# Kernel optimization log

Measured on AMD Instinct MI355X. Metric: run time of the kernel, lower is better.

The kernel has to match this reference:

```python
import jax, jax.numpy as jnp
import numpy as np

N_NODES = 50000
N_EDGES = 800000
D_IN = 128
D_OUT = 128


def setup_inputs() -> dict:
    key = jax.random.key(0)
    k1, k2, k3, k4, k5 = jax.random.split(key, 5)
    x = jax.random.normal(k1, (N_NODES, D_IN), dtype=jnp.float32)
    src = jax.random.randint(k2, (N_EDGES,), 0, N_NODES, dtype=jnp.int32)
    dst = jax.random.randint(k3, (N_EDGES,), 0, N_NODES, dtype=jnp.int32)
    # nn.Linear(in_feats, out_feats): weight [out, in], bias [out]
    W = jax.random.normal(k4, (D_OUT, D_IN), dtype=jnp.float32) / np.sqrt(D_IN)
    b = jax.random.normal(k5, (D_OUT,), dtype=jnp.float32) * 0.01
    return {"x": x, "src": src, "dst": dst, "W": W, "b": b}


def reference(x, src, dst, W, b):
    # copy_u('h','m') + sum reduce: h_dst = sum_{e:(u->v)} x[u]
    msgs = x[src]  # [E, D_IN] gather of source features
    h = jax.ops.segment_sum(msgs, dst, num_segments=N_NODES)  # [N, D_IN]
    # linear: h @ W.T + b ; dropout_rate=0.0 -> identity
    out = jnp.einsum('nd,od->no', h, W) + b
    return out
```

## Files before the change

kernel.cpp:

```cpp
#include <hip/hip_runtime.h>

#define N_NODES 50000
#define N_EDGES 800000
#define D 128
#define NB 782
#define SORT_CAP 2048

typedef __attribute__((ext_vector_type(8))) short bf16x8;
typedef __attribute__((ext_vector_type(4))) float floatx4;

__device__ __forceinline__ unsigned short f2bf(float f) {
  unsigned u = __builtin_bit_cast(unsigned, f);
  unsigned r = u + 0x7FFFu + ((u >> 16) & 1u);
  return (unsigned short)(r >> 16);
}
__device__ __forceinline__ float bf2f_lo(unsigned u) {
  return __builtin_bit_cast(float, u << 16);
}
__device__ __forceinline__ float bf2f_hi(unsigned u) {
  return __builtin_bit_cast(float, u & 0xFFFF0000u);
}

#define LDA 136
#define BIN_T 256
#define BIN_CHUNK 2048
#define BIN_BLOCKS 391

struct BinShm {
  unsigned stage[BIN_CHUNK];
  unsigned short stageb[BIN_CHUNK];
  int hcnt[NB];
  int hstart[NB];
  int hcur[NB];
  int hgbase[NB];
  int wsums[4];
  int tot;
};
struct GemmShm {
  unsigned short As[64 * LDA];
  unsigned short Ws[128 * LDA];
};
union PrepShm {
  BinShm bin;
  GemmShm gemm;
};

__global__ __launch_bounds__(256) void prep_kernel(
    const float* __restrict__ x, const float* __restrict__ W,
    unsigned short* __restrict__ y,
    const int* __restrict__ src, const int* __restrict__ dst,
    int* __restrict__ bcursor, unsigned* __restrict__ ebuf, int cap) {
  __shared__ PrepShm shm;
  int t = threadIdx.x;

  if (blockIdx.x < NB) {
    unsigned short* As = shm.gemm.As;
    unsigned short* Ws = shm.gemm.Ws;
    int row0 = blockIdx.x * 64;

    for (int i = t; i < 2048; i += 256) {
      int r = i >> 5;
      int c4 = (i & 31) * 4;
      int gr = row0 + r;
      float4 v = (gr < N_NODES) ? *(const float4*)(x + (size_t)gr * D + c4)
                                : float4{0.f, 0.f, 0.f, 0.f};
      unsigned short* p = &As[r * LDA + c4];
      p[0] = f2bf(v.x); p[1] = f2bf(v.y); p[2] = f2bf(v.z); p[3] = f2bf(v.w);
    }
    for (int i = t; i < 4096; i += 256) {
      int r = i >> 5;
      int c4 = (i & 31) * 4;
      float4 wv = *(const float4*)(W + (size_t)r * D + c4);
      unsigned short* q = &Ws[r * LDA + c4];
      q[0] = f2bf(wv.x); q[1] = f2bf(wv.y); q[2] = f2bf(wv.z); q[3] = f2bf(wv.w);
    }
    __syncthreads();

    int w = t >> 6;
    int lane = t & 63;
    int ln = lane & 15;
    int quad = lane >> 4;

    floatx4 acc[8];
#pragma unroll
    for (int n = 0; n < 8; ++n) acc[n] = floatx4{0.f, 0.f, 0.f, 0.f};

#pragma unroll
    for (int ks = 0; ks < 4; ++ks) {
      int kc = ks * 32 + quad * 8;
      bf16x8 a = *(const bf16x8*)&As[(w * 16 + ln) * LDA + kc];
#pragma unroll
      for (int n = 0; n < 8; ++n) {
        bf16x8 bf = *(const bf16x8*)&Ws[(n * 16 + ln) * LDA + kc];
        acc[n] = __builtin_amdgcn_mfma_f32_16x16x32_bf16(a, bf, acc[n], 0, 0, 0);
      }
    }

    int gr0 = row0 + w * 16 + quad * 4;
#pragma unroll
    for (int n = 0; n < 8; ++n) {
      int gc = n * 16 + ln;
#pragma unroll
      for (int r = 0; r < 4; ++r) {
        int gr = gr0 + r;
        if (gr < N_NODES) y[(size_t)gr * D + gc] = f2bf(acc[n][r]);
      }
    }
  } else {
    BinShm& B = shm.bin;
    int blk = blockIdx.x - NB;
    int e0 = blk * BIN_CHUNK;
    for (int i = t; i < NB; i += BIN_T) B.hcnt[i] = 0;
    __syncthreads();

    unsigned pk[8];
    short bk[8];
#pragma unroll
    for (int j = 0; j < 8; ++j) {
      int e = e0 + j * BIN_T + t;
      bk[j] = -1;
      if (e < N_EDGES) {
        int d = dst[e];
        int s = src[e];
        pk[j] = ((unsigned)s << 6) | (unsigned)(d & 63);
        bk[j] = (short)(d >> 6);
        atomicAdd(&B.hcnt[d >> 6], 1);
      }
    }
    __syncthreads();

    int c4[4];
    int s4 = 0;
    int base4 = t * 4;
#pragma unroll
    for (int j = 0; j < 4; ++j) {
      int idx = base4 + j;
      c4[j] = (idx < NB) ? B.hcnt[idx] : 0;
      s4 += c4[j];
    }
    int incl = s4;
    int lane = t & 63, wid = t >> 6;
#pragma unroll
    for (int off = 1; off < 64; off <<= 1) {
      int n = __shfl_up(incl, off);
      if (lane >= off) incl += n;
    }
    if (lane == 63) B.wsums[wid] = incl;
    __syncthreads();
    int wbase = 0;
    for (int w2 = 0; w2 < wid; ++w2) wbase += B.wsums[w2];
    int run = wbase + incl - s4;
#pragma unroll
    for (int j = 0; j < 4; ++j) {
      int idx = base4 + j;
      if (idx < NB) { B.hstart[idx] = run; B.hcur[idx] = run; }
      run += c4[j];
    }
    if (t == BIN_T - 1) B.tot = run;
    __syncthreads();

    for (int i = t; i < NB; i += BIN_T) {
      int c = B.hcnt[i];
      B.hgbase[i] = c ? atomicAdd(&bcursor[i * 16], c) : 0;
    }
#pragma unroll
    for (int j = 0; j < 8; ++j) {
      if (bk[j] >= 0) {
        int p = atomicAdd(&B.hcur[bk[j]], 1);
        B.stage[p] = pk[j];
        B.stageb[p] = (unsigned short)bk[j];
      }
    }
    __syncthreads();

    int tot = B.tot;
    for (int i = t; i < tot; i += BIN_T) {
      int b = B.stageb[i];
      int g = B.hgbase[b] + (i - B.hstart[b]);
      if (g < cap) ebuf[(size_t)b * cap + g] = B.stage[i];
    }
  }
}

__global__ __launch_bounds__(256) void gather_sorted(
    const unsigned short* __restrict__ y, const unsigned* __restrict__ ebuf,
    const int* __restrict__ bcursor, const float* __restrict__ bias,
    float* __restrict__ out, int cap) {
  __shared__ int cnts[64];
  __shared__ int curs[64];
  __shared__ int starts[65];
  __shared__ int sorted[SORT_CAP];

  int b = blockIdx.x;
  int t = threadIdx.x;
  if (t < 64) cnts[t] = 0;
  __syncthreads();

  int cnt = bcursor[b * 16];
  if (cnt > cap) cnt = cap;
  if (cnt > SORT_CAP) cnt = SORT_CAP;
  const unsigned* eb = ebuf + (size_t)b * cap;

  for (int i = t; i < cnt; i += 256) atomicAdd(&cnts[eb[i] & 63u], 1);
  __syncthreads();

  if (t < 64) {
    int c = cnts[t];
    int v = c;
#pragma unroll
    for (int off = 1; off < 64; off <<= 1) {
      int n = __shfl_up(v, off);
      if (t >= off) v += n;
    }
    starts[t] = v - c;
    curs[t] = v - c;
    if (t == 63) starts[64] = v;
  }
  __syncthreads();

  for (int i = t; i < cnt; i += 256) {
    unsigned u = eb[i];
    int p = atomicAdd(&curs[u & 63u], 1);
    sorted[p] = (int)(u >> 6);
  }
  __syncthreads();

  int wv = t >> 6;
  int lane = t & 63;
  int g = lane >> 4;
  int l = lane & 15;
  for (int n = wv; n < 64; n += 4) {
    int node = b * 64 + n;
    int beg = starts[n];
    int end = starts[n + 1];
    float acc[8] = {0.f, 0.f, 0.f, 0.f, 0.f, 0.f, 0.f, 0.f};
    int i = beg + g;
    for (; i + 12 < end; i += 16) {
      int s0 = sorted[i];
      int s1 = sorted[i + 4];
      int s2 = sorted[i + 8];
      int s3 = sorted[i + 12];
      uint4 u0 = *(const uint4*)(y + (size_t)s0 * D + l * 8);
      uint4 u1 = *(const uint4*)(y + (size_t)s1 * D + l * 8);
      uint4 u2 = *(const uint4*)(y + (size_t)s2 * D + l * 8);
      uint4 u3 = *(const uint4*)(y + (size_t)s3 * D + l * 8);
      acc[0] += (bf2f_lo(u0.x) + bf2f_lo(u1.x)) + (bf2f_lo(u2.x) + bf2f_lo(u3.x));
      acc[1] += (bf2f_hi(u0.x) + bf2f_hi(u1.x)) + (bf2f_hi(u2.x) + bf2f_hi(u3.x));
      acc[2] += (bf2f_lo(u0.y) + bf2f_lo(u1.y)) + (bf2f_lo(u2.y) + bf2f_lo(u3.y));
      acc[3] += (bf2f_hi(u0.y) + bf2f_hi(u1.y)) + (bf2f_hi(u2.y) + bf2f_hi(u3.y));
      acc[4] += (bf2f_lo(u0.z) + bf2f_lo(u1.z)) + (bf2f_lo(u2.z) + bf2f_lo(u3.z));
      acc[5] += (bf2f_hi(u0.z) + bf2f_hi(u1.z)) + (bf2f_hi(u2.z) + bf2f_hi(u3.z));
      acc[6] += (bf2f_lo(u0.w) + bf2f_lo(u1.w)) + (bf2f_lo(u2.w) + bf2f_lo(u3.w));
      acc[7] += (bf2f_hi(u0.w) + bf2f_hi(u1.w)) + (bf2f_hi(u2.w) + bf2f_hi(u3.w));
    }
    for (; i < end; i += 4) {
      int s = sorted[i];
      uint4 u = *(const uint4*)(y + (size_t)s * D + l * 8);
      acc[0] += bf2f_lo(u.x); acc[1] += bf2f_hi(u.x);
      acc[2] += bf2f_lo(u.y); acc[3] += bf2f_hi(u.y);
      acc[4] += bf2f_lo(u.z); acc[5] += bf2f_hi(u.z);
      acc[6] += bf2f_lo(u.w); acc[7] += bf2f_hi(u.w);
    }
#pragma unroll
    for (int j = 0; j < 8; ++j) {
      acc[j] += __shfl_xor(acc[j], 16);
      acc[j] += __shfl_xor(acc[j], 32);
    }
    if (g == 0 && node < N_NODES) {
      const float* bp = bias + l * 8;
      float4 r0 = {acc[0] + bp[0], acc[1] + bp[1], acc[2] + bp[2], acc[3] + bp[3]};
      float4 r1 = {acc[4] + bp[4], acc[5] + bp[5], acc[6] + bp[6], acc[7] + bp[7]};
      float* op = out + (size_t)node * D + l * 8;
      *(float4*)op = r0;
      *(float4*)(op + 4) = r1;
    }
  }
}

__global__ __launch_bounds__(256) void hist_kernel(
    const int* __restrict__ dst, int* __restrict__ counts) {
  int e = blockIdx.x * 256 + threadIdx.x;
  if (e < N_EDGES) atomicAdd(&counts[dst[e]], 1);
}

#define SBLK 196
__global__ __launch_bounds__(256) void reduce_kernel(
    const int* __restrict__ counts, int* __restrict__ blockSums) {
  int i = blockIdx.x * 256 + threadIdx.x;
  int v = (i < N_NODES) ? counts[i] : 0;
#pragma unroll
  for (int off = 32; off; off >>= 1) v += __shfl_down(v, off);
  __shared__ int ws[4];
  int lane = threadIdx.x & 63, wid = threadIdx.x >> 6;
  if (lane == 0) ws[wid] = v;
  __syncthreads();
  if (threadIdx.x == 0) blockSums[blockIdx.x] = ws[0] + ws[1] + ws[2] + ws[3];
}

__global__ __launch_bounds__(256) void scan_kernel2(
    const int* __restrict__ counts, const int* __restrict__ blockSums,
    int* __restrict__ offsets, int* __restrict__ cursor) {
  int b = blockIdx.x;
  int t = threadIdx.x;
  int lane = t & 63, wid = t >> 6;
  int pv = (t < b) ? blockSums[t] : 0;
#pragma unroll
  for (int off = 32; off; off >>= 1) pv += __shfl_down(pv, off);
  __shared__ int ws[4];
  __shared__ int wsum[4];
  __shared__ int base_s;
  if (lane == 0) ws[wid] = pv;
  __syncthreads();
  if (t == 0) base_s = ws[0] + ws[1] + ws[2] + ws[3];
  int i = b * 256 + t;
  int c = (i < N_NODES) ? counts[i] : 0;
  int v = c;
#pragma unroll
  for (int off = 1; off < 64; off <<= 1) {
    int n = __shfl_up(v, off);
    if (lane >= off) v += n;
  }
  if (lane == 63) wsum[wid] = v;
  __syncthreads();
  int wbase = 0;
  for (int w2 = 0; w2 < wid; ++w2) wbase += wsum[w2];
  int excl = base_s + wbase + v - c;
  if (i < N_NODES) {
    offsets[i] = excl;
    cursor[i] = excl;
    if (i == N_NODES - 1) offsets[N_NODES] = excl + c;
  }
}

__global__ __launch_bounds__(256) void fill_kernel(
    const int* __restrict__ src, const int* __restrict__ dst,
    int* __restrict__ cursor, int* __restrict__ esrc) {
  int e = blockIdx.x * 256 + threadIdx.x;
  if (e >= N_EDGES) return;
  int pos = atomicAdd(&cursor[dst[e]], 1);
  esrc[pos] = src[e];
}

__global__ __launch_bounds__(256) void gemm_xw(
    const float* __restrict__ x, const float* __restrict__ W,
    unsigned short* __restrict__ y) {
  __shared__ unsigned short As[64 * LDA];
  __shared__ unsigned short Ws[128 * LDA];
  int t = threadIdx.x;
  int row0 = blockIdx.x * 64;
  for (int i = t; i < 2048; i += 256) {
    int r = i >> 5;
    int c4 = (i & 31) * 4;
    int gr = row0 + r;
    float4 v = (gr < N_NODES) ? *(const float4*)(x + (size_t)gr * D + c4)
                              : float4{0.f, 0.f, 0.f, 0.f};
    unsigned short* p = &As[r * LDA + c4];
    p[0] = f2bf(v.x); p[1] = f2bf(v.y); p[2] = f2bf(v.z); p[3] = f2bf(v.w);
  }
  for (int i = t; i < 4096; i += 256) {
    int r = i >> 5;
    int c4 = (i & 31) * 4;
    float4 wv = *(const float4*)(W + (size_t)r * D + c4);
    unsigned short* q = &Ws[r * LDA + c4];
    q[0] = f2bf(wv.x); q[1] = f2bf(wv.y); q[2] = f2bf(wv.z); q[3] = f2bf(wv.w);
  }
  __syncthreads();
  int w = t >> 6;
  int lane = t & 63;
  int ln = lane & 15;
  int quad = lane >> 4;
  floatx4 acc[8];
#pragma unroll
  for (int n = 0; n < 8; ++n) acc[n] = floatx4{0.f, 0.f, 0.f, 0.f};
#pragma unroll
  for (int ks = 0; ks < 4; ++ks) {
    int kc = ks * 32 + quad * 8;
    bf16x8 a = *(const bf16x8*)&As[(w * 16 + ln) * LDA + kc];
#pragma unroll
    for (int n = 0; n < 8; ++n) {
      bf16x8 bf = *(const bf16x8*)&Ws[(n * 16 + ln) * LDA + kc];
      acc[n] = __builtin_amdgcn_mfma_f32_16x16x32_bf16(a, bf, acc[n], 0, 0, 0);
    }
  }
  int gr0 = row0 + w * 16 + quad * 4;
#pragma unroll
  for (int n = 0; n < 8; ++n) {
    int gc = n * 16 + ln;
#pragma unroll
    for (int r = 0; r < 4; ++r) {
      int gr = gr0 + r;
      if (gr < N_NODES) y[(size_t)gr * D + gc] = f2bf(acc[n][r]);
    }
  }
}

__global__ __launch_bounds__(256) void gather_ybf_kernel(
    const unsigned short* __restrict__ y, const int* __restrict__ esrc,
    const int* __restrict__ offsets, const float* __restrict__ bias,
    float* __restrict__ out) {
  int node = blockIdx.x * 4 + (threadIdx.x >> 6);
  if (node >= N_NODES) return;
  int lane = threadIdx.x & 63;
  int g = lane >> 4;
  int l = lane & 15;
  int beg = offsets[node];
  int end = offsets[node + 1];
  float acc[8] = {0.f, 0.f, 0.f, 0.f, 0.f, 0.f, 0.f, 0.f};
  int i = beg + g;
  for (; i + 4 < end; i += 8) {
    int s0 = esrc[i];
    int s1 = esrc[i + 4];
    uint4 u0 = *(const uint4*)(y + (size_t)s0 * D + l * 8);
    uint4 u1 = *(const uint4*)(y + (size_t)s1 * D + l * 8);
    acc[0] += bf2f_lo(u0.x) + bf2f_lo(u1.x);
    acc[1] += bf2f_hi(u0.x) + bf2f_hi(u1.x);
    acc[2] += bf2f_lo(u0.y) + bf2f_lo(u1.y);
    acc[3] += bf2f_hi(u0.y) + bf2f_hi(u1.y);
    acc[4] += bf2f_lo(u0.z) + bf2f_lo(u1.z);
    acc[5] += bf2f_hi(u0.z) + bf2f_hi(u1.z);
    acc[6] += bf2f_lo(u0.w) + bf2f_lo(u1.w);
    acc[7] += bf2f_hi(u0.w) + bf2f_hi(u1.w);
  }
  if (i < end) {
    int s = esrc[i];
    uint4 u = *(const uint4*)(y + (size_t)s * D + l * 8);
    acc[0] += bf2f_lo(u.x); acc[1] += bf2f_hi(u.x);
    acc[2] += bf2f_lo(u.y); acc[3] += bf2f_hi(u.y);
    acc[4] += bf2f_lo(u.z); acc[5] += bf2f_hi(u.z);
    acc[6] += bf2f_lo(u.w); acc[7] += bf2f_hi(u.w);
  }
#pragma unroll
  for (int j = 0; j < 8; ++j) {
    acc[j] += __shfl_xor(acc[j], 16);
    acc[j] += __shfl_xor(acc[j], 32);
  }
  if (g == 0) {
    const float* bp = bias + l * 8;
    float4 r0 = {acc[0] + bp[0], acc[1] + bp[1], acc[2] + bp[2], acc[3] + bp[3]};
    float4 r1 = {acc[4] + bp[4], acc[5] + bp[5], acc[6] + bp[6], acc[7] + bp[7]};
    float* op = out + (size_t)node * D + l * 8;
    *(float4*)op = r0;
    *(float4*)(op + 4) = r1;
  }
}

__global__ __launch_bounds__(256) void scatter_kernel(
    const float* __restrict__ x, const int* __restrict__ src,
    const int* __restrict__ dst, float* __restrict__ out) {
  int gtid = blockIdx.x * 256 + threadIdx.x;
  int e = gtid >> 6;
  int lane = threadIdx.x & 63;
  if (e >= N_EDGES) return;
  float2 v = ((const float2*)(x + (size_t)src[e] * D))[lane];
  float* orow = out + (size_t)dst[e] * D + lane * 2;
  atomicAdd(orow + 0, v.x);
  atomicAdd(orow + 1, v.y);
}

__global__ __launch_bounds__(256) void transform_kernel(
    float* __restrict__ out, const float* __restrict__ W,
    const float* __restrict__ bias) {
  constexpr int RPB = 64;
  constexpr int HP = 132;
  __shared__ float Hs[RPB][HP];
  int t = threadIdx.x;
  int row0 = blockIdx.x * RPB;
  int nr = min(RPB, N_NODES - row0);
  {
    const float4* g = (const float4*)(out + (size_t)row0 * D);
    for (int i = t; i < nr * (D / 4); i += 256) {
      int r = i >> 5;
      int c = (i & 31) * 4;
      *(float4*)&Hs[r][c] = g[i];
    }
  }
  __syncthreads();
  int tx = t & 15;
  int ty = t >> 4;
  int r0 = ty * 4;
  for (int half = 0; half < 2; ++half) {
    int oc0 = half * 64 + tx * 4;
    const float* Wb = W + (size_t)oc0 * D;
    float4 a0 = {0.f, 0.f, 0.f, 0.f}, a1 = {0.f, 0.f, 0.f, 0.f};
    float4 a2 = {0.f, 0.f, 0.f, 0.f}, a3 = {0.f, 0.f, 0.f, 0.f};
#pragma unroll 8
    for (int k = 0; k < D; k += 4) {
      float4 w0 = *(const float4*)(Wb + 0 * D + k);
      float4 w1 = *(const float4*)(Wb + 1 * D + k);
      float4 w2 = *(const float4*)(Wb + 2 * D + k);
      float4 w3 = *(const float4*)(Wb + 3 * D + k);
      float4 h0 = *(const float4*)&Hs[r0 + 0][k];
      float4 h1 = *(const float4*)&Hs[r0 + 1][k];
      float4 h2 = *(const float4*)&Hs[r0 + 2][k];
      float4 h3 = *(const float4*)&Hs[r0 + 3][k];
#define DOT(hv, wv) fmaf((hv).w, (wv).w, fmaf((hv).z, (wv).z, fmaf((hv).y, (wv).y, (hv).x * (wv).x)))
      a0.x += DOT(h0, w0); a0.y += DOT(h0, w1); a0.z += DOT(h0, w2); a0.w += DOT(h0, w3);
      a1.x += DOT(h1, w0); a1.y += DOT(h1, w1); a1.z += DOT(h1, w2); a1.w += DOT(h1, w3);
      a2.x += DOT(h2, w0); a2.y += DOT(h2, w1); a2.z += DOT(h2, w2); a2.w += DOT(h2, w3);
      a3.x += DOT(h3, w0); a3.y += DOT(h3, w1); a3.z += DOT(h3, w2); a3.w += DOT(h3, w3);
#undef DOT
    }
    float4 bv = *(const float4*)(bias + oc0);
    a0.x += bv.x; a0.y += bv.y; a0.z += bv.z; a0.w += bv.w;
    a1.x += bv.x; a1.y += bv.y; a1.z += bv.z; a1.w += bv.w;
    a2.x += bv.x; a2.y += bv.y; a2.z += bv.z; a2.w += bv.w;
    a3.x += bv.x; a3.y += bv.y; a3.z += bv.z; a3.w += bv.w;
    if (r0 + 0 < nr) *(float4*)(out + (size_t)(row0 + r0 + 0) * D + oc0) = a0;
    if (r0 + 1 < nr) *(float4*)(out + (size_t)(row0 + r0 + 1) * D + oc0) = a1;
    if (r0 + 2 < nr) *(float4*)(out + (size_t)(row0 + r0 + 2) * D + oc0) = a2;
    if (r0 + 3 < nr) *(float4*)(out + (size_t)(row0 + r0 + 3) * D + oc0) = a3;
  }
}

extern "C" void kernel_launch(void* const* d_in, const int* in_sizes, int n_in,
                              void* d_out, int out_size, void* d_ws, size_t ws_size,
                              hipStream_t stream) {
  const float* x = (const float*)d_in[0];
  const int* src = (const int*)d_in[1];
  const int* dst = (const int*)d_in[2];
  const float* W = (const float*)d_in[3];
  const float* b = (const float*)d_in[4];
  float* out = (float*)d_out;

  const size_t ybytes = (size_t)N_NODES * D * sizeof(unsigned short);
  const size_t bcbytes = (size_t)NB * 16 * sizeof(int);

  long long avail = (long long)ws_size - (long long)ybytes - (long long)bcbytes;
  int cap = 0;
  if (avail > 0) {
    long long c = avail / (4LL * NB);
    cap = (c > SORT_CAP) ? SORT_CAP : (int)c;
  }

  if (cap >= 1344) {
    unsigned short* y = (unsigned short*)d_ws;
    int* bcursor = (int*)((char*)d_ws + ybytes);
    unsigned* ebuf = (unsigned*)((char*)bcursor + bcbytes);

    hipMemsetAsync(bcursor, 0, bcbytes, stream);
    prep_kernel<<<NB + BIN_BLOCKS, 256, 0, stream>>>(x, W, y, src, dst,
                                                     bcursor, ebuf, cap);
    gather_sorted<<<NB, 256, 0, stream>>>(y, ebuf, bcursor, b, out, cap);
    return;
  }

  const size_t A = 50048;
  const size_t head_ints = 3 * A + 256 + (size_t)N_EDGES;
  const size_t need_csr = head_ints * sizeof(int) + ybytes;

  if (ws_size >= need_csr) {
    int* counts     = (int*)d_ws;
    int* offsets    = counts + A;
    int* cursor     = offsets + A;
    int* blockSums  = cursor + A;
    int* esrc       = blockSums + 256;
    unsigned short* y = (unsigned short*)(esrc + N_EDGES);

    hipMemsetAsync(counts, 0, N_NODES * sizeof(int), stream);
    hist_kernel<<<(N_EDGES + 255) / 256, 256, 0, stream>>>(dst, counts);
    reduce_kernel<<<SBLK, 256, 0, stream>>>(counts, blockSums);
    scan_kernel2<<<SBLK, 256, 0, stream>>>(counts, blockSums, offsets, cursor);
    fill_kernel<<<(N_EDGES + 255) / 256, 256, 0, stream>>>(src, dst, cursor, esrc);
    gemm_xw<<<NB, 256, 0, stream>>>(x, W, y);
    gather_ybf_kernel<<<(N_NODES + 3) / 4, 256, 0, stream>>>(y, esrc, offsets, b, out);
  } else {
    hipMemsetAsync(out, 0, (size_t)N_NODES * D * sizeof(float), stream);
    scatter_kernel<<<N_EDGES / 4, 256, 0, stream>>>(x, src, dst, out);
    transform_kernel<<<(N_NODES + 63) / 64, 256, 0, stream>>>(out, W, b);
  }
}
```

Before: 149.9 us.

## Replace global atomic bucket scatter with per-block sorted segments and offset table

```diff
diff --git a/kernel.cpp b/kernel.cpp
--- a/kernel.cpp
+++ b/kernel.cpp
@@ -23,16 +23,15 @@
 
 #define LDA 136
 #define BIN_T 256
-#define BIN_CHUNK 2048
-#define BIN_BLOCKS 391
+#define BIN_CHUNK 4096
+#define BIN_BLOCKS 196
+#define OFFS_W 783
 
 struct BinShm {
   unsigned stage[BIN_CHUNK];
-  unsigned short stageb[BIN_CHUNK];
   int hcnt[NB];
   int hstart[NB];
   int hcur[NB];
-  int hgbase[NB];
   int wsums[4];
   int tot;
 };
@@ -49,14 +48,14 @@
     const float* __restrict__ x, const float* __restrict__ W,
     unsigned short* __restrict__ y,
     const int* __restrict__ src, const int* __restrict__ dst,
-    int* __restrict__ bcursor, unsigned* __restrict__ ebuf, int cap) {
+    unsigned* __restrict__ ebuf, int* __restrict__ offs) {
   __shared__ PrepShm shm;
   int t = threadIdx.x;
 
-  if (blockIdx.x < NB) {
+  if (blockIdx.x >= BIN_BLOCKS) {
     unsigned short* As = shm.gemm.As;
     unsigned short* Ws = shm.gemm.Ws;
-    int row0 = blockIdx.x * 64;
+    int row0 = (blockIdx.x - BIN_BLOCKS) * 64;
 
     for (int i = t; i < 2048; i += 256) {
       int r = i >> 5;
@@ -108,15 +107,15 @@
     }
   } else {
     BinShm& B = shm.bin;
-    int blk = blockIdx.x - NB;
+    int blk = blockIdx.x;
     int e0 = blk * BIN_CHUNK;
     for (int i = t; i < NB; i += BIN_T) B.hcnt[i] = 0;
     __syncthreads();
 
-    unsigned pk[8];
-    short bk[8];
-#pragma unroll
-    for (int j = 0; j < 8; ++j) {
+    unsigned pk[16];
+    short bk[16];
+#pragma unroll
+    for (int j = 0; j < 16; ++j) {
       int e = e0 + j * BIN_T + t;
       bk[j] = -1;
       if (e < N_EDGES) {
@@ -159,76 +158,104 @@
     if (t == BIN_T - 1) B.tot = run;
     __syncthreads();
 
-    for (int i = t; i < NB; i += BIN_T) {
-      int c = B.hcnt[i];
-      B.hgbase[i] = c ? atomicAdd(&bcursor[i * 16], c) : 0;
-    }
-#pragma unroll
-    for (int j = 0; j < 8; ++j) {
+#pragma unroll
+    for (int j = 0; j < 16; ++j) {
       if (bk[j] >= 0) {
         int p = atomicAdd(&B.hcur[bk[j]], 1);
         B.stage[p] = pk[j];
-        B.stageb[p] = (unsigned short)bk[j];
       }
     }
     __syncthreads();
 
     int tot = B.tot;
-    for (int i = t; i < tot; i += BIN_T) {
-      int b = B.stageb[i];
-      int g = B.hgbase[b] + (i - B.hstart[b]);
-      if (g < cap) ebuf[(size_t)b * cap + g] = B.stage[i];
-    }
+    unsigned* dseg = ebuf + (size_t)blk * BIN_CHUNK;
+    int tot4 = tot >> 2;
+    uint4* d4 = (uint4*)dseg;
+    const uint4* s4p = (const uint4*)B.stage;
+    for (int i = t; i < tot4; i += BIN_T) d4[i] = s4p[i];
+    for (int i = (tot & ~3) + t; i < tot; i += BIN_T) dseg[i] = B.stage[i];
+
+    int* orow = offs + (size_t)blk * OFFS_W;
+    for (int i = t; i < NB; i += BIN_T) orow[i] = B.hstart[i];
+    if (t == 0) orow[NB] = tot;
   }
 }
 
 __global__ __launch_bounds__(256) void gather_sorted(
     const unsigned short* __restrict__ y, const unsigned* __restrict__ ebuf,
-    const int* __restrict__ bcursor, const float* __restrict__ bias,
-    float* __restrict__ out, int cap) {
+    const int* __restrict__ offs, const float* __restrict__ bias,
+    float* __restrict__ out) {
   __shared__ int cnts[64];
   __shared__ int curs[64];
   __shared__ int starts[65];
   __shared__ int sorted[SORT_CAP];
+  __shared__ unsigned ec[SORT_CAP];
+  __shared__ int wsum2[4];
+  __shared__ int segtot;
 
   int b = blockIdx.x;
   int t = threadIdx.x;
   if (t < 64) cnts[t] = 0;
-  __syncthreads();
-
-  int cnt = bcursor[b * 16];
-  if (cnt > cap) cnt = cap;
+
+  int s0 = 0, slen = 0;
+  if (t < BIN_BLOCKS) {
+    const int* orow = offs + (size_t)t * OFFS_W;
+    s0 = orow[b];
+    slen = orow[b + 1] - s0;
+  }
+  int lane = t & 63, wid = t >> 6;
+  int v = slen;
+#pragma unroll
+  for (int off = 1; off < 64; off <<= 1) {
+    int n = __shfl_up(v, off);
+    if (lane >= off) v += n;
+  }
+  if (lane == 63) wsum2[wid] = v;
+  __syncthreads();
+  int wbase = 0;
+  for (int w2 = 0; w2 < wid; ++w2) wbase += wsum2[w2];
+  int base = wbase + v - slen;
+  if (t == 255) segtot = wbase + v;
+
+  const unsigned* myseg = ebuf + (size_t)t * BIN_CHUNK + s0;
+  for (int j = 0; j < slen; ++j) {
+    int p = base + j;
+    if (p < SORT_CAP) ec[p] = myseg[j];
+  }
+  __syncthreads();
+
+  int cnt = segtot;
   if (cnt > SORT_CAP) cnt = SORT_CAP;
-  const unsigned* eb = ebuf + (size_t)b * cap;
-
-  for (int i = t; i < cnt; i += 256) atomicAdd(&cnts[eb[i] & 63u], 1);
+
+  for (int i = t; i < cnt; i += 256) atomicAdd(&cnts[ec[i] & 63u], 1);
   __syncthreads();
 
   if (t < 64) {
     int c = cnts[t];
-    int v = c;
+    int vv = c;
 #pragma unroll
     for (int off = 1; off < 64; off <<= 1) {
-      int n = __shfl_up(v, off);
-      if (t >= off) v += n;
-    }
-    starts[t] = v - c;
-    curs[t] = v - c;
-    if (t == 63) starts[64] = v;
+      int n = __shfl_up(vv, off);
+      if (t >= off) vv += n;
+    }
+    starts[t] = vv - c;
+    curs[t] = vv - c;
+    if (t == 63) starts[64] = vv;
   }
   __syncthreads();
 
   for (int i = t; i < cnt; i += 256) {
-    unsigned u = eb[i];
+    unsigned u = ec[i];
     int p = atomicAdd(&curs[u & 63u], 1);
     sorted[p] = (int)(u >> 6);
   }
   __syncthreads();
 
   int wv = t >> 6;
-  int lane = t & 63;
   int g = lane >> 4;
   int l = lane & 15;
+  float4 bv0 = *(const float4*)(bias + l * 8);
+  float4 bv1 = *(const float4*)(bias + l * 8 + 4);
   for (int n = wv; n < 64; n += 4) {
     int node = b * 64 + n;
     int beg = starts[n];
@@ -236,14 +263,14 @@
     float acc[8] = {0.f, 0.f, 0.f, 0.f, 0.f, 0.f, 0.f, 0.f};
     int i = beg + g;
     for (; i + 12 < end; i += 16) {
-      int s0 = sorted[i];
-      int s1 = sorted[i + 4];
-      int s2 = sorted[i + 8];
-      int s3 = sorted[i + 12];
-      uint4 u0 = *(const uint4*)(y + (size_t)s0 * D + l * 8);
-      uint4 u1 = *(const uint4*)(y + (size_t)s1 * D + l * 8);
-      uint4 u2 = *(const uint4*)(y + (size_t)s2 * D + l * 8);
-      uint4 u3 = *(const uint4*)(y + (size_t)s3 * D + l * 8);
+      int s0e = sorted[i];
+      int s1e = sorted[i + 4];
+      int s2e = sorted[i + 8];
+      int s3e = sorted[i + 12];
+      uint4 u0 = *(const uint4*)(y + (size_t)s0e * D + l * 8);
+      uint4 u1 = *(const uint4*)(y + (size_t)s1e * D + l * 8);
+      uint4 u2 = *(const uint4*)(y + (size_t)s2e * D + l * 8);
+      uint4 u3 = *(const uint4*)(y + (size_t)s3e * D + l * 8);
       acc[0] += (bf2f_lo(u0.x) + bf2f_lo(u1.x)) + (bf2f_lo(u2.x) + bf2f_lo(u3.x));
       acc[1] += (bf2f_hi(u0.x) + bf2f_hi(u1.x)) + (bf2f_hi(u2.x) + bf2f_hi(u3.x));
       acc[2] += (bf2f_lo(u0.y) + bf2f_lo(u1.y)) + (bf2f_lo(u2.y) + bf2f_lo(u3.y));
@@ -267,9 +294,8 @@
       acc[j] += __shfl_xor(acc[j], 32);
     }
     if (g == 0 && node < N_NODES) {
-      const float* bp = bias + l * 8;
-      float4 r0 = {acc[0] + bp[0], acc[1] + bp[1], acc[2] + bp[2], acc[3] + bp[3]};
-      float4 r1 = {acc[4] + bp[4], acc[5] + bp[5], acc[6] + bp[6], acc[7] + bp[7]};
+      float4 r0 = {acc[0] + bv0.x, acc[1] + bv0.y, acc[2] + bv0.z, acc[3] + bv0.w};
+      float4 r1 = {acc[4] + bv1.x, acc[5] + bv1.y, acc[6] + bv1.z, acc[7] + bv1.w};
       float* op = out + (size_t)node * D + l * 8;
       *(float4*)op = r0;
       *(float4*)(op + 4) = r1;
@@ -523,24 +549,16 @@
   float* out = (float*)d_out;
 
   const size_t ybytes = (size_t)N_NODES * D * sizeof(unsigned short);
-  const size_t bcbytes = (size_t)NB * 16 * sizeof(int);
-
-  long long avail = (long long)ws_size - (long long)ybytes - (long long)bcbytes;
-  int cap = 0;
-  if (avail > 0) {
-    long long c = avail / (4LL * NB);
-    cap = (c > SORT_CAP) ? SORT_CAP : (int)c;
-  }
-
-  if (cap >= 1344) {
+  const size_t ebytes = (size_t)BIN_BLOCKS * BIN_CHUNK * sizeof(unsigned);
+  const size_t obytes = (size_t)BIN_BLOCKS * OFFS_W * sizeof(int);
+
+  if (ws_size >= ybytes + ebytes + obytes) {
     unsigned short* y = (unsigned short*)d_ws;
-    int* bcursor = (int*)((char*)d_ws + ybytes);
-    unsigned* ebuf = (unsigned*)((char*)bcursor + bcbytes);
-
-    hipMemsetAsync(bcursor, 0, bcbytes, stream);
-    prep_kernel<<<NB + BIN_BLOCKS, 256, 0, stream>>>(x, W, y, src, dst,
-                                                     bcursor, ebuf, cap);
-    gather_sorted<<<NB, 256, 0, stream>>>(y, ebuf, bcursor, b, out, cap);
+    unsigned* ebuf = (unsigned*)((char*)d_ws + ybytes);
+    int* offs = (int*)((char*)ebuf + ebytes);
+
+    prep_kernel<<<BIN_BLOCKS + NB, 256, 0, stream>>>(x, W, y, src, dst, ebuf, offs);
+    gather_sorted<<<NB, 256, 0, stream>>>(y, ebuf, offs, b, out);
     return;
   }
 
```

Result: faster. 140.1 us (-6.5%).
